# Performance work log

Measured on AMD Instinct MI355X. Metric: run time of the kernel, lower is better.

The kernel has to match this reference:

```python
import jax, jax.numpy as jnp
import numpy as np

T, B, H = 1024, 256, 20


def setup_inputs() -> dict:
    key = jax.random.key(0)
    ks = jax.random.split(key, 6)

    def lin_w(k, fan_in, fan_out):
        bound = 1.0 / np.sqrt(fan_in)
        return jax.random.uniform(k, (fan_in, fan_out), jnp.float32, -bound, bound)

    # t is time-reversed (torch.flip): strictly decreasing, so dt = t[0]-t[1] > 0
    t = jnp.linspace(1.0, 0.0, T, dtype=jnp.float32).reshape(T, 1)
    y = jax.random.uniform(ks[0], (B, 1, 3), jnp.float32)  # initial SIR state per batch
    return {
        "t": t,
        "y": y,
        "w1": lin_w(ks[1], 1, H), "b1": jnp.zeros((H,), jnp.float32),
        "w2": lin_w(ks[2], H, H), "b2": jnp.zeros((H,), jnp.float32),
        "w3": lin_w(ks[3], H, H), "b3": jnp.zeros((H,), jnp.float32),
        "w4": lin_w(ks[4], H, 1), "b4": jnp.zeros((1,), jnp.float32),
        "beta": jnp.asarray(0.2, jnp.float32),
        "gamma": jnp.asarray(0.2, jnp.float32),
    }


def reference(t, y, w1, b1, w2, b2, w3, b3, w4, b4, beta, gamma):
    Tn = t.shape[0]
    dt = t[0, 0] - t[1, 0]  # positive scalar (t is reversed)

    # memory kernel me(t): Linear-Tanh x3 -> Linear-Sigmoid, shape [T]
    h = jnp.tanh(t @ w1 + b1)
    h = jnp.tanh(h @ w2 + b2)
    h = jnp.tanh(h @ w3 + b3)
    me = jax.nn.sigmoid(h @ w4 + b4)[:, 0]  # [T]
    # pad so me[-j:] can be read as a fixed-length dynamic slice (zeros past end)
    me_pad = jnp.concatenate([me, jnp.zeros((Tn,), me.dtype)])  # [2T]

    y0 = jnp.transpose(y, (1, 0, 2))[0]  # [B,3]  (y.transpose(1,0) then first/only row)
    Bn = y0.shape[0]
    # history buffer of I-compartment values; entries >= current length stay zero
    I_hist0 = jnp.zeros((Tn, Bn), y0.dtype).at[0].set(y0[:, 1])

    def step(carry, idx):
        y_cur, I_hist = carry  # y_cur [B,3], I_hist [T,B]
        j = idx + 1  # current solution length
        # kernel slice w[k] = me[T - j + k]; for k >= j both w (padding) and I_hist are 0
        w = jax.lax.dynamic_slice(me_pad, (Tn - j,), (Tn,))  # [T]
        integ = dt * jnp.einsum('t,tb->b', w, I_hist)  # memory integral, [B]
        S, I = y_cur[:, 0], y_cur[:, 1]
        bSI = beta * S * I
        gI = gamma * I
        d = jnp.stack([-bSI + integ, bSI - gI, gI - integ], axis=1)  # [B,3]
        y_next = y_cur + d * dt  # forward Euler
        I_hist = I_hist.at[j].set(y_next[:, 1])
        return (y_next, I_hist), (d, y_next)

    (_, _), (ds, ys) = jax.lax.scan(step, (y0, I_hist0), jnp.arange(Tn - 1))
    solution = jnp.concatenate([y0[None], ys], axis=0)  # [T,B,3]
    # original leaves diff[T-1] as zeros (loop fills rows 0..T-2)
    diff = jnp.concatenate([ds, jnp.zeros((1, Bn, 3), ds.dtype)], axis=0)  # [T,B,3]
    return solution, diff
```

## Files before the change

kernel.cpp:

```cpp
#include <hip/hip_runtime.h>

#define T_N 1024
#define B_N 256
#define H_N 20
#define NW  8
#define NDW (NW - 1)
#define SIH 1096

typedef _Float16 h8_t __attribute__((ext_vector_type(8)));

#if __has_builtin(__builtin_amdgcn_fdot2)
#define DOT8(acc, mv, iv)                                                           \
    acc = __builtin_amdgcn_fdot2(__builtin_shufflevector(mv, mv, 0, 1),             \
                                 __builtin_shufflevector(iv, iv, 0, 1), acc, false);\
    acc = __builtin_amdgcn_fdot2(__builtin_shufflevector(mv, mv, 2, 3),             \
                                 __builtin_shufflevector(iv, iv, 2, 3), acc, false);\
    acc = __builtin_amdgcn_fdot2(__builtin_shufflevector(mv, mv, 4, 5),             \
                                 __builtin_shufflevector(iv, iv, 4, 5), acc, false);\
    acc = __builtin_amdgcn_fdot2(__builtin_shufflevector(mv, mv, 6, 7),             \
                                 __builtin_shufflevector(iv, iv, 6, 7), acc, false);
#else
#define DOT8(acc, mv, iv)                                                           \
    _Pragma("unroll")                                                               \
    for (int _k = 0; _k < 8; ++_k) acc = fmaf((float)mv[_k], (float)iv[_k], acc);
#endif

__device__ __forceinline__ float rdlane_i(float v, int lane) {
    return __uint_as_float((unsigned)__builtin_amdgcn_readlane((int)__float_as_uint(v), lane));
}
__device__ __forceinline__ float fast_tanh(float x) {
    const float e = __expf(2.0f * x);
    return fmaf(-2.0f, __builtin_amdgcn_rcpf(e + 1.0f), 1.0f);
}
__device__ __forceinline__ float fast_sigmoid(float x) {
    return __builtin_amdgcn_rcpf(1.0f + __expf(-x));
}

#define REP64(F) \
    F(0) F(1) F(2) F(3) F(4) F(5) F(6) F(7) F(8) F(9) F(10) F(11) F(12) F(13) \
    F(14) F(15) F(16) F(17) F(18) F(19) F(20) F(21) F(22) F(23) F(24) F(25)   \
    F(26) F(27) F(28) F(29) F(30) F(31) F(32) F(33) F(34) F(35) F(36) F(37)   \
    F(38) F(39) F(40) F(41) F(42) F(43) F(44) F(45) F(46) F(47) F(48) F(49)   \
    F(50) F(51) F(52) F(53) F(54) F(55) F(56) F(57) F(58) F(59) F(60) F(61)   \
    F(62) F(63)

__global__ __launch_bounds__(512, 1) void scan_kernel(
    const float* __restrict__ t,
    const float* __restrict__ y,
    const float* __restrict__ w1, const float* __restrict__ b1,
    const float* __restrict__ w2, const float* __restrict__ b2,
    const float* __restrict__ w3, const float* __restrict__ b3,
    const float* __restrict__ w4, const float* __restrict__ b4,
    const float* __restrict__ beta_p,
    const float* __restrict__ gamma_p,
    float* __restrict__ out)
{
    __shared__ __align__(16) float    sMeF[T_N];
    __shared__ __align__(16) _Float16 sMeH[T_N];
    __shared__ __align__(16) _Float16 sIhR[8 * SIH];
    __shared__ float P[2][NDW][64];

    const int b   = blockIdx.x;
    const int tid = threadIdx.x;
    const int wid = tid >> 6;
    const int L   = tid & 63;

    const int f    = (-L) & 7;
    const int R8   = L + f;
    const int row  = L & 7;
    const int iofs = row * SIH + (f ? 0 : 8);

    if (tid < 64) sIhR[(tid >> 3) * SIH + (tid & 7)] = (_Float16)0.0f;

#pragma unroll
    for (int v = 0; v < 2; ++v) {
        const int mi = tid + v * 512;
        const float x = t[mi];

        float h1[H_N], h2[H_N];
#pragma unroll
        for (int k = 0; k < H_N; ++k) h1[k] = fast_tanh(fmaf(x, w1[k], b1[k]));

#pragma unroll 4
        for (int k = 0; k < H_N; ++k) {
            float a = b2[k];
#pragma unroll
            for (int j = 0; j < H_N; ++j) a = fmaf(h1[j], w2[j * H_N + k], a);
            h2[k] = fast_tanh(a);
        }

        float a4 = b4[0];
#pragma unroll 4
        for (int k = 0; k < H_N; ++k) {
            float a = b3[k];
#pragma unroll
            for (int j = 0; j < H_N; ++j) a = fmaf(h2[j], w3[j * H_N + k], a);
            a4 = fmaf(fast_tanh(a), w4[k], a4);
        }

        const float meval = fast_sigmoid(a4);
        sMeF[mi] = meval;
        sMeH[mi] = (_Float16)meval;
    }

    const float dt    = t[0] - t[1];
    const float beta  = beta_p[0];
    const float gma   = gamma_p[0];
    const float invdt = 1.0f / dt;

    const float S0 = y[b * 3 + 0];
    const float I0 = y[b * 3 + 1];
    const float R0 = y[b * 3 + 2];
    const float TOT = S0 + I0 + R0;

    if (tid < 8) sIhR[tid * SIH + 8 - tid] = (_Float16)I0;

    float* __restrict__ diff = out + (size_t)T_N * B_N * 3;
    if (tid < 3) diff[((size_t)(T_N - 1) * B_N + b) * 3 + tid] = 0.0f;

    __syncthreads();

    float mf[7];
#pragma unroll
    for (int d = 1; d <= 7; ++d) mf[d - 1] = sMeF[T_N - 64 - L - d];

    const float dtb  = dt * beta;
    const float ndtg = -dt * gma;
    const float dt2  = dt * dt;
    const float meT1 = sMeF[T_N - 1];

    float S = S0, I = I0, oS = S0, oI = I0;
    float acc_cur = 0.0f, acc_nxt = 0.0f, pre = 0.0f;
    float carryS = S0, carryI = I0;

#define TBLDECL(k) float rm_##k, rn_##k;
    REP64(TBLDECL)
#undef TBLDECL
    if (wid == 0) {
#define TBLINIT(k)                                                      \
        rm_##k = ((k) < L) ? sMeF[T_N - L + (k)] : 0.0f;                \
        rn_##k = sMeF[T_N - 64 - L + (k)];
        REP64(TBLINIT)
#undef TBLINIT
#define TBLPIN(k) asm volatile("" : "+v"(rm_##k), "+v"(rn_##k));
        REP64(TBLPIN)
#undef TBLPIN
    }

#define STEPB(M_, FIRST_)                                               \
    {                                                                   \
        const float sum = (FIRST_) ? pre : fmaf(meT1, I, pre);          \
        float pnx = pre;                                                \
        if ((M_) < 63) pnx = rdlane_i(acc_cur, (M_) + 1);               \
        const float bI = dtb * I;                                       \
        const float i1 = fmaf(ndtg, I, I);                              \
        const float q  = bI * S;                                        \
        const float s1 = S - q;                                         \
        S = fmaf(dt2, sum, s1);                                         \
        I = i1 + q;                                                     \
        const bool cap = (L == (M_));                                   \
        oS = cap ? S : oS;                                              \
        oI = cap ? I : oI;                                              \
        acc_cur = fmaf(rm_##M_, I, acc_cur);                            \
        acc_nxt = fmaf(rn_##M_, I, acc_nxt);                            \
        pre = pnx;                                                      \
    }
#define STEP_GE1(M_) if ((M_) >= 1) STEPB(M_, false)
#define STEP_GE2(M_) if ((M_) >= 2) STEPB(M_, false)

    for (int c = 0; c < 16; ++c) {
        if (wid == 0) {
            if (c == 0) {
                acc_cur = rm_0 * I;
                acc_nxt = rn_0 * I;
                pre = rdlane_i(acc_cur, 1);
                STEPB(1, true)
                REP64(STEP_GE2)
            } else {
                float ac = acc_nxt;
#pragma unroll
                for (int w = 0; w < NDW; ++w) ac += P[c & 1][w][L];
                acc_cur = ac;
                acc_nxt = 0.0f;
                pre = rdlane_i(acc_cur, 0);
                STEPB(0, true)
                REP64(STEP_GE1)
            }

            const int j = 64 * c + L;
            const _Float16 hI = (_Float16)oI;
#pragma unroll
            for (int r = 0; r < 8; ++r) sIhR[r * SIH + 8 + (j - r)] = hI;

            const float oR = TOT - oS - oI;
            const size_t so = ((size_t)j * B_N + b) * 3;
            out[so + 0] = oS;
            out[so + 1] = oI;
            out[so + 2] = oR;

            float sm1 = __shfl_up(oS, 1);
            float im1 = __shfl_up(oI, 1);
            if (L == 0) { sm1 = carryS; im1 = carryI; }
            if (j > 0) {
                const float d0 = (oS - sm1) * invdt;
                const float d1 = (oI - im1) * invdt;
                const float d2 = -d0 - d1;
                const size_t dofs = ((size_t)(j - 1) * B_N + b) * 3;
                diff[dofs + 0] = d0;
                diff[dofs + 1] = d1;
                diff[dofs + 2] = d2;
            }
            carryS = rdlane_i(oS, 63);
            carryI = rdlane_i(oI, 63);
        } else if (c < 15) {
            const int w    = wid - 1;
            const int G    = 8 * c;
            const int idx0 = (T_N - 64 * (c + 1)) - R8;
            float p0 = 0.0f, p1 = 0.0f;
            int s = w;
            for (; s + NDW < G; s += 2 * NDW) {
                const h8_t mv0 = *(const h8_t*)&sMeH[idx0 + 8 * s];
                const h8_t iv0 = *(const h8_t*)&sIhR[iofs + 8 * s];
                const h8_t mv1 = *(const h8_t*)&sMeH[idx0 + 8 * (s + NDW)];
                const h8_t iv1 = *(const h8_t*)&sIhR[iofs + 8 * (s + NDW)];
                DOT8(p0, mv0, iv0)
                DOT8(p1, mv1, iv1)
            }
            if (s < G) {
                const h8_t mv0 = *(const h8_t*)&sMeH[idx0 + 8 * s];
                const h8_t iv0 = *(const h8_t*)&sIhR[iofs + 8 * s];
                DOT8(p0, mv0, iv0)
            }
            float p = p0 + p1;
            if (w == 0) {
#pragma unroll
                for (int d = 1; d <= 7; ++d) {
                    const float ih = (float)sIhR[8 + 64 * c - d];
                    if (d <= f) p = fmaf(mf[d - 1], ih, p);
                }
            }
            P[(c + 1) & 1][w][L] = p;
        }
        __syncthreads();
    }
#undef STEPB
#undef STEP_GE1
#undef STEP_GE2
}

extern "C" void kernel_launch(void* const* d_in, const int* in_sizes, int n_in,
                              void* d_out, int out_size, void* d_ws, size_t ws_size,
                              hipStream_t stream) {
    const float* t     = (const float*)d_in[0];
    const float* y     = (const float*)d_in[1];
    const float* w1    = (const float*)d_in[2];
    const float* b1    = (const float*)d_in[3];
    const float* w2    = (const float*)d_in[4];
    const float* b2    = (const float*)d_in[5];
    const float* w3    = (const float*)d_in[6];
    const float* b3    = (const float*)d_in[7];
    const float* w4    = (const float*)d_in[8];
    const float* b4    = (const float*)d_in[9];
    const float* beta  = (const float*)d_in[10];
    const float* gamma = (const float*)d_in[11];

    scan_kernel<<<B_N, 512, 0, stream>>>(t, y, w1, b1, w2, b2, w3, b3, w4, b4,
                                         beta, gamma, (float*)d_out);
}
```

Baseline: 121.8 us.

## Process two batch elements per block to interleave independent serial recurrences

Each block now handles two batch elements, so the grid shrinks to 128 blocks and wave 0 advances two independent Euler recurrences in lockstep. This gives the latency-bound serial chain two independent instruction streams to overlap, and the helper waves share one memory-kernel load across two history dot products. The update is also rewritten algebraically, with dt² folded into the register tables and the S/I updates reduced to FMA forms. The cost is roughly double the register pressure in wave 0, which already holds 128 table registers, and only half the CUs are occupied on a 256-CU device.

```diff
diff --git a/kernel.cpp b/kernel.cpp
--- a/kernel.cpp
+++ b/kernel.cpp
@@ -57,10 +57,12 @@
 {
     __shared__ __align__(16) float    sMeF[T_N];
     __shared__ __align__(16) _Float16 sMeH[T_N];
-    __shared__ __align__(16) _Float16 sIhR[8 * SIH];
-    __shared__ float P[2][NDW][64];
-
-    const int b   = blockIdx.x;
+    __shared__ __align__(16) _Float16 sIhR0[8 * SIH];
+    __shared__ __align__(16) _Float16 sIhR1[8 * SIH];
+    __shared__ float P[2][2][NDW][64];
+
+    const int b0  = blockIdx.x * 2;
+    const int b1i = b0 + 1;
     const int tid = threadIdx.x;
     const int wid = tid >> 6;
     const int L   = tid & 63;
@@ -70,7 +72,10 @@
     const int row  = L & 7;
     const int iofs = row * SIH + (f ? 0 : 8);
 
-    if (tid < 64) sIhR[(tid >> 3) * SIH + (tid & 7)] = (_Float16)0.0f;
+    if (tid < 64) {
+        sIhR0[(tid >> 3) * SIH + (tid & 7)] = (_Float16)0.0f;
+        sIhR1[(tid >> 3) * SIH + (tid & 7)] = (_Float16)0.0f;
+    }
 
 #pragma unroll
     for (int v = 0; v < 2; ++v) {
@@ -107,16 +112,28 @@
     const float beta  = beta_p[0];
     const float gma   = gamma_p[0];
     const float invdt = 1.0f / dt;
-
-    const float S0 = y[b * 3 + 0];
-    const float I0 = y[b * 3 + 1];
-    const float R0 = y[b * 3 + 2];
-    const float TOT = S0 + I0 + R0;
-
-    if (tid < 8) sIhR[tid * SIH + 8 - tid] = (_Float16)I0;
+    const float dt2   = dt * dt;
+
+    const float S00 = y[b0 * 3 + 0];
+    const float I00 = y[b0 * 3 + 1];
+    const float R00 = y[b0 * 3 + 2];
+    const float TOT0 = S00 + I00 + R00;
+
+    const float S10 = y[b1i * 3 + 0];
+    const float I10 = y[b1i * 3 + 1];
+    const float R10 = y[b1i * 3 + 2];
+    const float TOT1 = S10 + I10 + R10;
+
+    if (tid < 8) {
+        sIhR0[tid * SIH + 8 - tid] = (_Float16)I00;
+        sIhR1[tid * SIH + 8 - tid] = (_Float16)I10;
+    }
 
     float* __restrict__ diff = out + (size_t)T_N * B_N * 3;
-    if (tid < 3) diff[((size_t)(T_N - 1) * B_N + b) * 3 + tid] = 0.0f;
+    if (tid < 6) {
+        const int bb = (tid >= 3) ? b1i : b0;
+        diff[((size_t)(T_N - 1) * B_N + bb) * 3 + (tid % 3)] = 0.0f;
+    }
 
     __syncthreads();
 
@@ -124,22 +141,25 @@
 #pragma unroll
     for (int d = 1; d <= 7; ++d) mf[d - 1] = sMeF[T_N - 64 - L - d];
 
-    const float dtb  = dt * beta;
-    const float ndtg = -dt * gma;
-    const float dt2  = dt * dt;
-    const float meT1 = sMeF[T_N - 1];
-
-    float S = S0, I = I0, oS = S0, oI = I0;
-    float acc_cur = 0.0f, acc_nxt = 0.0f, pre = 0.0f;
-    float carryS = S0, carryI = I0;
+    const float dtb   = dt * beta;
+    const float ndtb  = -dtb;
+    const float c1    = fmaf(-dt, gma, 1.0f);
+    const float meT1s = dt2 * sMeF[T_N - 1];
+
+    float S0v = S00, I0v = I00, oS0 = S00, oI0 = I00;
+    float S1v = S10, I1v = I10, oS1 = S10, oI1 = I10;
+    float acc_cur0 = 0.0f, acc_nxt0 = 0.0f, pre0 = 0.0f;
+    float acc_cur1 = 0.0f, acc_nxt1 = 0.0f, pre1 = 0.0f;
+    float carryS0 = S00, carryI0 = I00;
+    float carryS1 = S10, carryI1 = I10;
 
 #define TBLDECL(k) float rm_##k, rn_##k;
     REP64(TBLDECL)
 #undef TBLDECL
     if (wid == 0) {
-#define TBLINIT(k)                                                      \
-        rm_##k = ((k) < L) ? sMeF[T_N - L + (k)] : 0.0f;                \
-        rn_##k = sMeF[T_N - 64 - L + (k)];
+#define TBLINIT(k)                                                          \
+        rm_##k = (((k) < L) ? sMeF[T_N - L + (k)] : 0.0f) * dt2;            \
+        rn_##k = dt2 * sMeF[T_N - 64 - L + (k)];
         REP64(TBLINIT)
 #undef TBLINIT
 #define TBLPIN(k) asm volatile("" : "+v"(rm_##k), "+v"(rn_##k));
@@ -149,21 +169,32 @@
 
 #define STEPB(M_, FIRST_)                                               \
     {                                                                   \
-        const float sum = (FIRST_) ? pre : fmaf(meT1, I, pre);          \
-        float pnx = pre;                                                \
-        if ((M_) < 63) pnx = rdlane_i(acc_cur, (M_) + 1);               \
-        const float bI = dtb * I;                                       \
-        const float i1 = fmaf(ndtg, I, I);                              \
-        const float q  = bI * S;                                        \
-        const float s1 = S - q;                                         \
-        S = fmaf(dt2, sum, s1);                                         \
-        I = i1 + q;                                                     \
+        const float sum0 = (FIRST_) ? pre0 : fmaf(meT1s, I0v, pre0);    \
+        const float sum1 = (FIRST_) ? pre1 : fmaf(meT1s, I1v, pre1);    \
+        float pnx0 = pre0, pnx1 = pre1;                                 \
+        if ((M_) < 63) {                                                \
+            pnx0 = rdlane_i(acc_cur0, (M_) + 1);                        \
+            pnx1 = rdlane_i(acc_cur1, (M_) + 1);                        \
+        }                                                               \
+        const float a0 = fmaf(dtb, S0v, c1);                            \
+        const float a1 = fmaf(dtb, S1v, c1);                            \
+        const float bb0 = fmaf(ndtb, I0v, 1.0f);                        \
+        const float bb1 = fmaf(ndtb, I1v, 1.0f);                        \
+        S0v = fmaf(bb0, S0v, sum0);                                     \
+        S1v = fmaf(bb1, S1v, sum1);                                     \
+        I0v = I0v * a0;                                                 \
+        I1v = I1v * a1;                                                 \
         const bool cap = (L == (M_));                                   \
-        oS = cap ? S : oS;                                              \
-        oI = cap ? I : oI;                                              \
-        acc_cur = fmaf(rm_##M_, I, acc_cur);                            \
-        acc_nxt = fmaf(rn_##M_, I, acc_nxt);                            \
-        pre = pnx;                                                      \
+        oS0 = cap ? S0v : oS0;                                          \
+        oI0 = cap ? I0v : oI0;                                          \
+        oS1 = cap ? S1v : oS1;                                          \
+        oI1 = cap ? I1v : oI1;                                          \
+        acc_cur0 = fmaf(rm_##M_, I0v, acc_cur0);                        \
+        acc_nxt0 = fmaf(rn_##M_, I0v, acc_nxt0);                        \
+        acc_cur1 = fmaf(rm_##M_, I1v, acc_cur1);                        \
+        acc_nxt1 = fmaf(rn_##M_, I1v, acc_nxt1);                        \
+        pre0 = pnx0;                                                    \
+        pre1 = pnx1;                                                    \
     }
 #define STEP_GE1(M_) if ((M_) >= 1) STEPB(M_, false)
 #define STEP_GE2(M_) if ((M_) >= 2) STEPB(M_, false)
@@ -171,75 +202,110 @@
     for (int c = 0; c < 16; ++c) {
         if (wid == 0) {
             if (c == 0) {
-                acc_cur = rm_0 * I;
-                acc_nxt = rn_0 * I;
-                pre = rdlane_i(acc_cur, 1);
+                acc_cur0 = rm_0 * I0v;  acc_nxt0 = rn_0 * I0v;
+                acc_cur1 = rm_0 * I1v;  acc_nxt1 = rn_0 * I1v;
+                pre0 = rdlane_i(acc_cur0, 1);
+                pre1 = rdlane_i(acc_cur1, 1);
                 STEPB(1, true)
                 REP64(STEP_GE2)
             } else {
-                float ac = acc_nxt;
-#pragma unroll
-                for (int w = 0; w < NDW; ++w) ac += P[c & 1][w][L];
-                acc_cur = ac;
-                acc_nxt = 0.0f;
-                pre = rdlane_i(acc_cur, 0);
+                float ps0 = 0.0f, ps1 = 0.0f;
+#pragma unroll
+                for (int w = 0; w < NDW; ++w) {
+                    ps0 += P[c & 1][0][w][L];
+                    ps1 += P[c & 1][1][w][L];
+                }
+                acc_cur0 = fmaf(dt2, ps0, acc_nxt0);
+                acc_cur1 = fmaf(dt2, ps1, acc_nxt1);
+                acc_nxt0 = 0.0f;
+                acc_nxt1 = 0.0f;
+                pre0 = rdlane_i(acc_cur0, 0);
+                pre1 = rdlane_i(acc_cur1, 0);
                 STEPB(0, true)
                 REP64(STEP_GE1)
             }
 
             const int j = 64 * c + L;
-            const _Float16 hI = (_Float16)oI;
-#pragma unroll
-            for (int r = 0; r < 8; ++r) sIhR[r * SIH + 8 + (j - r)] = hI;
-
-            const float oR = TOT - oS - oI;
-            const size_t so = ((size_t)j * B_N + b) * 3;
-            out[so + 0] = oS;
-            out[so + 1] = oI;
-            out[so + 2] = oR;
-
-            float sm1 = __shfl_up(oS, 1);
-            float im1 = __shfl_up(oI, 1);
-            if (L == 0) { sm1 = carryS; im1 = carryI; }
+            const _Float16 hI0 = (_Float16)oI0;
+            const _Float16 hI1 = (_Float16)oI1;
+#pragma unroll
+            for (int r = 0; r < 8; ++r) sIhR0[r * SIH + 8 + (j - r)] = hI0;
+#pragma unroll
+            for (int r = 0; r < 8; ++r) sIhR1[r * SIH + 8 + (j - r)] = hI1;
+
+            const float oR0 = TOT0 - oS0 - oI0;
+            const float oR1 = TOT1 - oS1 - oI1;
+            const size_t so0 = ((size_t)j * B_N + b0) * 3;
+            out[so0 + 0] = oS0;
+            out[so0 + 1] = oI0;
+            out[so0 + 2] = oR0;
+            out[so0 + 3] = oS1;
+            out[so0 + 4] = oI1;
+            out[so0 + 5] = oR1;
+
+            float sm10 = __shfl_up(oS0, 1);
+            float im10 = __shfl_up(oI0, 1);
+            float sm11 = __shfl_up(oS1, 1);
+            float im11 = __shfl_up(oI1, 1);
+            if (L == 0) { sm10 = carryS0; im10 = carryI0; sm11 = carryS1; im11 = carryI1; }
             if (j > 0) {
-                const float d0 = (oS - sm1) * invdt;
-                const float d1 = (oI - im1) * invdt;
-                const float d2 = -d0 - d1;
-                const size_t dofs = ((size_t)(j - 1) * B_N + b) * 3;
-                diff[dofs + 0] = d0;
-                diff[dofs + 1] = d1;
-                diff[dofs + 2] = d2;
-            }
-            carryS = rdlane_i(oS, 63);
-            carryI = rdlane_i(oI, 63);
+                const float d00 = (oS0 - sm10) * invdt;
+                const float d01 = (oI0 - im10) * invdt;
+                const float d10 = (oS1 - sm11) * invdt;
+                const float d11 = (oI1 - im11) * invdt;
+                const size_t dofs = ((size_t)(j - 1) * B_N + b0) * 3;
+                diff[dofs + 0] = d00;
+                diff[dofs + 1] = d01;
+                diff[dofs + 2] = -d00 - d01;
+                diff[dofs + 3] = d10;
+                diff[dofs + 4] = d11;
+                diff[dofs + 5] = -d10 - d11;
+            }
+            carryS0 = rdlane_i(oS0, 63);
+            carryI0 = rdlane_i(oI0, 63);
+            carryS1 = rdlane_i(oS1, 63);
+            carryI1 = rdlane_i(oI1, 63);
         } else if (c < 15) {
             const int w    = wid - 1;
             const int G    = 8 * c;
             const int idx0 = (T_N - 64 * (c + 1)) - R8;
-            float p0 = 0.0f, p1 = 0.0f;
+            float p00 = 0.0f, p01 = 0.0f;
+            float p10 = 0.0f, p11 = 0.0f;
             int s = w;
             for (; s + NDW < G; s += 2 * NDW) {
-                const h8_t mv0 = *(const h8_t*)&sMeH[idx0 + 8 * s];
-                const h8_t iv0 = *(const h8_t*)&sIhR[iofs + 8 * s];
-                const h8_t mv1 = *(const h8_t*)&sMeH[idx0 + 8 * (s + NDW)];
-                const h8_t iv1 = *(const h8_t*)&sIhR[iofs + 8 * (s + NDW)];
-                DOT8(p0, mv0, iv0)
-                DOT8(p1, mv1, iv1)
+                const h8_t mv0  = *(const h8_t*)&sMeH[idx0 + 8 * s];
+                const h8_t mv1  = *(const h8_t*)&sMeH[idx0 + 8 * (s + NDW)];
+                const h8_t iva0 = *(const h8_t*)&sIhR0[iofs + 8 * s];
+                const h8_t iva1 = *(const h8_t*)&sIhR0[iofs + 8 * (s + NDW)];
+                const h8_t ivb0 = *(const h8_t*)&sIhR1[iofs + 8 * s];
+                const h8_t ivb1 = *(const h8_t*)&sIhR1[iofs + 8 * (s + NDW)];
+                DOT8(p00, mv0, iva0)
+                DOT8(p01, mv1, iva1)
+                DOT8(p10, mv0, ivb0)
+                DOT8(p11, mv1, ivb1)
             }
             if (s < G) {
-                const h8_t mv0 = *(const h8_t*)&sMeH[idx0 + 8 * s];
-                const h8_t iv0 = *(const h8_t*)&sIhR[iofs + 8 * s];
-                DOT8(p0, mv0, iv0)
-            }
-            float p = p0 + p1;
+                const h8_t mv0  = *(const h8_t*)&sMeH[idx0 + 8 * s];
+                const h8_t iva0 = *(const h8_t*)&sIhR0[iofs + 8 * s];
+                const h8_t ivb0 = *(const h8_t*)&sIhR1[iofs + 8 * s];
+                DOT8(p00, mv0, iva0)
+                DOT8(p10, mv0, ivb0)
+            }
+            float p0 = p00 + p01;
+            float p1 = p10 + p11;
             if (w == 0) {
 #pragma unroll
                 for (int d = 1; d <= 7; ++d) {
-                    const float ih = (float)sIhR[8 + 64 * c - d];
-                    if (d <= f) p = fmaf(mf[d - 1], ih, p);
+                    const float ih0 = (float)sIhR0[8 + 64 * c - d];
+                    const float ih1 = (float)sIhR1[8 + 64 * c - d];
+                    if (d <= f) {
+                        p0 = fmaf(mf[d - 1], ih0, p0);
+                        p1 = fmaf(mf[d - 1], ih1, p1);
+                    }
                 }
             }
-            P[(c + 1) & 1][w][L] = p;
+            P[(c + 1) & 1][0][w][L] = p0;
+            P[(c + 1) & 1][1][w][L] = p1;
         }
         __syncthreads();
     }
@@ -264,6 +330,6 @@
     const float* beta  = (const float*)d_in[10];
     const float* gamma = (const float*)d_in[11];
 
-    scan_kernel<<<B_N, 512, 0, stream>>>(t, y, w1, b1, w2, b2, w3, b3, w4, b4,
-                                         beta, gamma, (float*)d_out);
-}
+    scan_kernel<<<B_N / 2, 512, 0, stream>>>(t, y, w1, b1, w2, b2, w3, b3, w4, b4,
+                                             beta, gamma, (float*)d_out);
+}
```

Measured after the change: 133.2 us. 9.4% more time.

## Shorten serial Euler dependency chain with prescaled weights and two-step lookahead

Applied to the files above, without the earlier changes.

Folds dt^2 into the per-lane memory-kernel weight tables and the meT1/meT2 constants, and refactors the S/I update into factored FMA forms (S*(1-dtb*I)+sum, I*(1+dtb*S-dt*g)). It also reads the lane-broadcast partial sum two steps ahead, adding the two newest history terms explicitly, so the cross-lane read leaves the critical path. The goal is fewer dependent instructions per sequential step in the wave-0 recurrence. The cost is an extra register and FMA per step, and slightly different float rounding.

```diff
diff --git a/kernel.cpp b/kernel.cpp
--- a/kernel.cpp
+++ b/kernel.cpp
@@ -107,6 +107,7 @@
     const float beta  = beta_p[0];
     const float gma   = gamma_p[0];
     const float invdt = 1.0f / dt;
+    const float dt2   = dt * dt;
 
     const float S0 = y[b * 3 + 0];
     const float I0 = y[b * 3 + 1];
@@ -124,22 +125,24 @@
 #pragma unroll
     for (int d = 1; d <= 7; ++d) mf[d - 1] = sMeF[T_N - 64 - L - d];
 
-    const float dtb  = dt * beta;
-    const float ndtg = -dt * gma;
-    const float dt2  = dt * dt;
-    const float meT1 = sMeF[T_N - 1];
-
-    float S = S0, I = I0, oS = S0, oI = I0;
-    float acc_cur = 0.0f, acc_nxt = 0.0f, pre = 0.0f;
+    const float dtb   = dt * beta;
+    const float ndtb  = -dtb;
+    const float c1    = fmaf(-dt, gma, 1.0f);
+    const float meT1s = dt2 * sMeF[T_N - 1];
+    const float meT2s = dt2 * sMeF[T_N - 2];
+
+    float S = S0, I = I0, Iprev = 0.0f, oS = S0, oI = I0;
+    float acc_cur = 0.0f, acc_nxt = 0.0f;
+    float pre_cur = 0.0f, pre_nxt = 0.0f;
     float carryS = S0, carryI = I0;
 
 #define TBLDECL(k) float rm_##k, rn_##k;
     REP64(TBLDECL)
 #undef TBLDECL
     if (wid == 0) {
-#define TBLINIT(k)                                                      \
-        rm_##k = ((k) < L) ? sMeF[T_N - L + (k)] : 0.0f;                \
-        rn_##k = sMeF[T_N - 64 - L + (k)];
+#define TBLINIT(k)                                                          \
+        rm_##k = (((k) < L) ? sMeF[T_N - L + (k)] : 0.0f) * dt2;            \
+        rn_##k = dt2 * sMeF[T_N - 64 - L + (k)];
         REP64(TBLINIT)
 #undef TBLINIT
 #define TBLPIN(k) asm volatile("" : "+v"(rm_##k), "+v"(rn_##k));
@@ -147,44 +150,53 @@
 #undef TBLPIN
     }
 
-#define STEPB(M_, FIRST_)                                               \
+#define STEPC(M_, NP_)                                                  \
     {                                                                   \
-        const float sum = (FIRST_) ? pre : fmaf(meT1, I, pre);          \
-        float pnx = pre;                                                \
-        if ((M_) < 63) pnx = rdlane_i(acc_cur, (M_) + 1);               \
-        const float bI = dtb * I;                                       \
-        const float i1 = fmaf(ndtg, I, I);                              \
-        const float q  = bI * S;                                        \
-        const float s1 = S - q;                                         \
-        S = fmaf(dt2, sum, s1);                                         \
-        I = i1 + q;                                                     \
+        float sum;                                                      \
+        if ((NP_) == 0)      sum = pre_cur;                             \
+        else if ((NP_) == 1) sum = fmaf(meT1s, I, pre_cur);             \
+        else                 sum = fmaf(meT1s, I, fmaf(meT2s, Iprev, pre_cur)); \
+        float rdv = pre_nxt;                                            \
+        if ((M_) + 2 <= 63) rdv = rdlane_i(acc_cur, (M_) + 2);          \
+        const float a  = fmaf(dtb, S, c1);                              \
+        const float bb = fmaf(ndtb, I, 1.0f);                           \
+        const float Sn = fmaf(bb, S, sum);                              \
+        const float In = I * a;                                         \
         const bool cap = (L == (M_));                                   \
-        oS = cap ? S : oS;                                              \
-        oI = cap ? I : oI;                                              \
-        acc_cur = fmaf(rm_##M_, I, acc_cur);                            \
-        acc_nxt = fmaf(rn_##M_, I, acc_nxt);                            \
-        pre = pnx;                                                      \
-    }
-#define STEP_GE1(M_) if ((M_) >= 1) STEPB(M_, false)
-#define STEP_GE2(M_) if ((M_) >= 2) STEPB(M_, false)
+        oS = cap ? Sn : oS;                                             \
+        oI = cap ? In : oI;                                             \
+        acc_cur = fmaf(rm_##M_, In, acc_cur);                           \
+        acc_nxt = fmaf(rn_##M_, In, acc_nxt);                           \
+        Iprev = I;                                                      \
+        I = In;                                                         \
+        S = Sn;                                                         \
+        pre_cur = pre_nxt;                                              \
+        pre_nxt = rdv;                                                  \
+    }
+#define STEP_GE2(M_) if ((M_) >= 2) STEPC(M_, 2)
+#define STEP_GE3(M_) if ((M_) >= 3) STEPC(M_, 2)
 
     for (int c = 0; c < 16; ++c) {
         if (wid == 0) {
             if (c == 0) {
                 acc_cur = rm_0 * I;
                 acc_nxt = rn_0 * I;
-                pre = rdlane_i(acc_cur, 1);
-                STEPB(1, true)
+                pre_cur = rdlane_i(acc_cur, 1);
+                pre_nxt = rdlane_i(acc_cur, 2);
+                STEPC(1, 0)
+                STEPC(2, 1)
+                REP64(STEP_GE3)
+            } else {
+                float ps = 0.0f;
+#pragma unroll
+                for (int w = 0; w < NDW; ++w) ps += P[c & 1][w][L];
+                acc_cur = fmaf(dt2, ps, acc_nxt);
+                acc_nxt = 0.0f;
+                pre_cur = rdlane_i(acc_cur, 0);
+                pre_nxt = rdlane_i(acc_cur, 1);
+                STEPC(0, 0)
+                STEPC(1, 1)
                 REP64(STEP_GE2)
-            } else {
-                float ac = acc_nxt;
-#pragma unroll
-                for (int w = 0; w < NDW; ++w) ac += P[c & 1][w][L];
-                acc_cur = ac;
-                acc_nxt = 0.0f;
-                pre = rdlane_i(acc_cur, 0);
-                STEPB(0, true)
-                REP64(STEP_GE1)
             }
 
             const int j = 64 * c + L;
@@ -243,9 +255,9 @@
         }
         __syncthreads();
     }
-#undef STEPB
-#undef STEP_GE1
+#undef STEPC
 #undef STEP_GE2
+#undef STEP_GE3
 }
 
 extern "C" void kernel_launch(void* const* d_in, const int* in_sizes, int n_in,
```

After: 122.6 us. No clear change (+0.7%).
